# Performance work log

Measured on AMD Instinct MI355X. Metric: run time of the kernel, lower is better.

Reference implementation:

```python
import jax, jax.numpy as jnp
import numpy as np

NTYPES = 2
NATOMS = (512, 512)
N = 1024          # total atoms
NN = 128          # neighbors per type
M = NTYPES * NN   # 256 neighbor slots per atom
D = 25            # last embedding width
FH = 240          # fitting hidden width
B = 8
RMIN, RMAX = 5.8, 6.0


def _embed_mlp(s, W0, b0, W1, b1, W2, b2):
    # DeepMD-style resnet embedding net: 1 -> D -> D -> D, tanh + skip
    h = jnp.tanh(s @ W0 + b0)
    h = h + jnp.tanh(h @ W1 + b1)
    h = h + jnp.tanh(h @ W2 + b2)
    return h


def setup_inputs() -> dict:
    key = jax.random.key(0)
    ks = jax.random.split(key, 20)
    # relative positions; components in [-4.5, 4.5] so |r| spans <5.8, [5.8,6.0), >=6.0
    image_dR = (jax.random.uniform(ks[0], (B, N, NTYPES, NN, 3), jnp.float32) - 0.5) * 9.0
    # 0 == empty neighbor slot (mask = list_neigh > 0); index-1 in [0, N)
    list_neigh = jax.random.randint(ks[1], (B, N, NTYPES, NN), 0, 1025)
    davg = 0.1 * jax.random.normal(ks[2], (NTYPES, M, 4), jnp.float32)
    dstd = jax.random.uniform(ks[3], (NTYPES, M, 4), jnp.float32, 0.5, 1.5)
    P = NTYPES * NTYPES
    eW0 = jax.random.normal(ks[4], (P, 1, D), jnp.float32)
    eb0 = 0.1 * jax.random.normal(ks[5], (P, D), jnp.float32)
    eW1 = jax.random.normal(ks[6], (P, D, D), jnp.float32) / np.sqrt(D)
    eb1 = 0.1 * jax.random.normal(ks[7], (P, D), jnp.float32)
    eW2 = jax.random.normal(ks[8], (P, D, D), jnp.float32) / np.sqrt(D)
    eb2 = 0.1 * jax.random.normal(ks[9], (P, D), jnp.float32)
    fW0 = jax.random.normal(ks[10], (NTYPES, 16 * D, FH), jnp.float32) / np.sqrt(16 * D)
    fb0 = 0.1 * jax.random.normal(ks[11], (NTYPES, FH), jnp.float32)
    fW1 = jax.random.normal(ks[12], (NTYPES, FH, FH), jnp.float32) / np.sqrt(FH)
    fb1 = 0.1 * jax.random.normal(ks[13], (NTYPES, FH), jnp.float32)
    fW2 = jax.random.normal(ks[14], (NTYPES, FH, FH), jnp.float32) / np.sqrt(FH)
    fb2 = 0.1 * jax.random.normal(ks[15], (NTYPES, FH), jnp.float32)
    fW3 = jax.random.normal(ks[16], (NTYPES, FH, 1), jnp.float32) / np.sqrt(FH)
    fb3 = 0.1 * jax.random.normal(ks[17], (NTYPES, 1), jnp.float32)
    ener_shift = 0.01 * jax.random.normal(ks[18], (NTYPES,), jnp.float32)
    return {
        'image_dR': image_dR, 'list_neigh': list_neigh,
        'davg': davg, 'dstd': dstd,
        'eW0': eW0, 'eb0': eb0, 'eW1': eW1, 'eb1': eb1, 'eW2': eW2, 'eb2': eb2,
        'fW0': fW0, 'fb0': fb0, 'fW1': fW1, 'fb1': fb1, 'fW2': fW2, 'fb2': fb2,
        'fW3': fW3, 'fb3': fb3, 'ener_shift': ener_shift,
        'dfeat': jnp.zeros((1,), jnp.float32),
        'Egroup_weight': jnp.zeros((1,), jnp.float32),
        'divider': jnp.ones((1,), jnp.float32),
    }


def _forward(image_dR, list_neigh, davg, dstd,
             eW0, eb0, eW1, eb1, eW2, eb2,
             fW0, fb0, fW1, fb1, fW2, fb2, fW3, fb3, ener_shift):
    dR = image_dR.reshape(B, N, M, 3)
    neigh = list_neigh.reshape(B, N, M)
    mask = neigh > 0
    mf = mask.astype(dR.dtype)
    dR2 = jnp.sum(dR * dR, axis=-1)                       # [B,N,M]
    safe_dR2 = jnp.where(mask, dR2, 1.0)
    Rij = jnp.sqrt(safe_dR2)
    inr = mf / Rij                                        # 1/|r|, 0 off-mask
    x = Rij * mf                                          # nr = dR2/Rij = |r|
    Ri_xyz = dR / safe_dR2[..., None] * mf[..., None]     # r / |r|^2
    inr2 = inr * inr
    inr4 = inr2 * inr2
    inr3 = inr4 * x
    # smooth switching function on [RMIN, RMAX]
    u = (x - RMIN) / (RMAX - RMIN)
    poly = u * u * u * (-6.0 * u * u + 15.0 * u - 10.0) + 1.0
    dpoly = (3.0 * u * u * (-6.0 * u * u + 15.0 * u - 10.0)
             + u * u * u * (-12.0 * u + 15.0)) / (RMAX - RMIN)
    mid = (x >= RMIN) & (x < RMAX)
    vv = jnp.where(x < RMIN, 1.0, jnp.where(mid, poly, 0.0)) * mf
    dvv = jnp.where(mid, dpoly, 0.0) * mf
    Ri_pre = jnp.concatenate([inr[..., None], Ri_xyz], axis=-1)   # [B,N,M,4]
    common = (dvv * inr)[..., None] * dR                          # [B,N,M,3]
    row0 = dR * (inr3 * vv)[..., None] - Ri_pre[..., 0:1] * common
    eye = jnp.eye(3, dtype=dR.dtype)
    outer = (2.0 * dR[..., :, None] * dR[..., None, :] * inr4[..., None, None]
             - eye * inr2[..., None, None])                       # [B,N,M,3,3]
    rows = outer * vv[..., None, None] - Ri_pre[..., 1:4, None] * common[..., None, :]
    Ri_d = jnp.concatenate([row0[..., None, :], rows], axis=-2) * mf[..., None, None]  # [B,N,M,4,3]
    Ri = Ri_pre * vv[..., None]
    # per-type normalization stats broadcast over atoms of each type
    davg_res = jnp.concatenate([jnp.broadcast_to(davg[t], (NATOMS[t], M, 4)) for t in range(NTYPES)], axis=0)
    dstd_res = jnp.concatenate([jnp.broadcast_to(dstd[t], (NATOMS[t], M, 4)) for t in range(NTYPES)], axis=0)
    Ri = (Ri - davg_res) / dstd_res
    Ri_d = Ri_d / dstd_res[..., None]

    def ei_fn(Ri_n):
        Ei_list = []
        start = 0
        for t in range(NTYPES):
            na = NATOMS[t]
            Rt = jax.lax.slice_in_dim(Ri_n, start, start + na, axis=1)  # [B,na,M,4]
            acc = jnp.zeros((B, na, 4, D), Ri_n.dtype)
            for t1 in range(NTYPES):
                p = t * NTYPES + t1
                blk = Rt[:, :, t1 * NN:(t1 + 1) * NN]                  # [B,na,NN,4]
                G = _embed_mlp(blk[..., 0:1], eW0[p], eb0[p], eW1[p], eb1[p], eW2[p], eb2[p])
                acc = acc + jnp.einsum('bnkd,bnke->bnde', blk, G)
            acc = acc * (4.0 / (NN * NTYPES * 4))
            DRt = jnp.einsum('bnde,bndf->bnef', acc, acc[..., :16]).reshape(B, na, D * 16)
            h = jnp.tanh(DRt @ fW0[t] + fb0[t])
            h = h + jnp.tanh(h @ fW1[t] + fb1[t])
            h = h + jnp.tanh(h @ fW2[t] + fb2[t])
            Ei_list.append(h @ fW3[t] + fb3[t] + ener_shift[t])
            start += na
        return jnp.concatenate(Ei_list, axis=1)   # [B,N,1]

    Ei, vjpf = jax.vjp(ei_fn, Ri)
    dE, = vjpf(jnp.ones_like(Ei))                 # dEi/dRi  [B,N,M,4]
    Etot = jnp.sum(Ei, axis=1)                    # [B,1]
    pair = jnp.einsum('bnmd,bnmdx->bnmx', dE, Ri_d)   # per-pair force term [B,N,M,3]
    F_self = -jnp.sum(pair, axis=2)
    j = neigh - 1
    valid = j >= 0
    flat_idx = jnp.where(valid, j, N) + jnp.arange(B)[:, None, None] * (N + 1)
    contrib = jnp.where(valid[..., None], pair, 0.0)
    seg = jax.ops.segment_sum(contrib.reshape(-1, 3), flat_idx.reshape(-1), num_segments=B * (N + 1))
    F = F_self + seg.reshape(B, N + 1, 3)[:, :N]
    return Etot, Ei, F


def reference(image_dR, list_neigh, davg, dstd,
              eW0, eb0, eW1, eb1, eW2, eb2,
              fW0, fb0, fW1, fb1, fW2, fb2, fW3, fb3, ener_shift,
              dfeat, Egroup_weight, divider):
    # dfeat / Egroup_weight / divider are in the torch forward signature but unused
    return _forward(image_dR, list_neigh, davg, dstd,
                    eW0, eb0, eW1, eb1, eW2, eb2,
                    fW0, fb0, fW1, fb1, fW2, fb2, fW3, fb3, ener_shift)
```

## Files before the change

kernel.cpp:

```cpp
#include <hip/hip_runtime.h>

#define DEV __device__ __forceinline__

#define RA(F) F(0) F(1) F(2) F(3) F(4) F(5) F(6) F(7) F(8) F(9) F(10) F(11) \
  F(12) F(13) F(14) F(15) F(16) F(17) F(18) F(19) F(20) F(21) F(22) F(23) F(24)
#define RB(F,j) F(j,0) F(j,1) F(j,2) F(j,3) F(j,4) F(j,5) F(j,6) F(j,7) F(j,8) \
  F(j,9) F(j,10) F(j,11) F(j,12) F(j,13) F(j,14) F(j,15) F(j,16) F(j,17) \
  F(j,18) F(j,19) F(j,20) F(j,21) F(j,22) F(j,23) F(j,24)
#define AP8(F) F(0) F(1) F(2) F(3) F(4) F(5) F(6) F(7)

namespace {

constexpr int B_ = 8;
constexpr int N_ = 1024;
constexpr int M_ = 256;
constexpr int D_ = 25;
constexpr int FH_ = 240;
constexpr int NATOM = B_ * N_;
constexpr float CSC = 1.0f / 256.0f;

DEV float fast_tanh(float x) {
  float ax = fabsf(x);
  float e = __expf(-2.0f * ax);
  float r = (1.0f - e) * __builtin_amdgcn_rcpf(1.0f + e);
  return copysignf(r, x);
}

DEV void geom_blk(float dx, float dy, float dz, int nb, int t, int m,
                  const float* __restrict__ davg, const float* __restrict__ dstd,
                  float& o0, float& o1, float& o2, float& o3) {
  float mf = (nb > 0) ? 1.0f : 0.0f;
  float dr2 = dx * dx + dy * dy + dz * dz;
  float safe = (nb > 0) ? dr2 : 1.0f;
  float rs = __builtin_amdgcn_rsqf(safe);
  float rij = safe * rs;
  float inr = mf * rs;
  float x = rij * mf;
  float inr2 = inr * inr;
  float u = (x - 5.8f) * 5.0f;
  float uu = u * u;
  float A = -6.0f * uu + 15.0f * u - 10.0f;
  float poly = uu * u * A + 1.0f;
  bool mid = (x >= 5.8f) && (x < 6.0f);
  float vv = ((x < 5.8f) ? 1.0f : (mid ? poly : 0.0f)) * mf;
  int bidx = (t * M_ + m) * 4;
  float4 av = *(const float4*)(davg + bidx);
  float4 sv = *(const float4*)(dstd + bidx);
  o0 = (inr * vv - av.x) * __builtin_amdgcn_rcpf(sv.x);
  o1 = (dx * inr2 * vv - av.y) * __builtin_amdgcn_rcpf(sv.y);
  o2 = (dy * inr2 * vv - av.z) * __builtin_amdgcn_rcpf(sv.z);
  o3 = (dz * inr2 * vv - av.w) * __builtin_amdgcn_rcpf(sv.w);
}

DEV void geom_force(float dx, float dy, float dz, int nb, int t, int m,
                    const float* __restrict__ dstd,
                    float dE0, float dE1, float dE2, float dE3,
                    float& px, float& py, float& pz) {
  float mf = (nb > 0) ? 1.0f : 0.0f;
  float dr2 = dx * dx + dy * dy + dz * dz;
  float safe = (nb > 0) ? dr2 : 1.0f;
  float rs = __builtin_amdgcn_rsqf(safe);
  float rij = safe * rs;
  float inr = mf * rs;
  float x = rij * mf;
  float inr2 = inr * inr;
  float inr4 = inr2 * inr2;
  float inr3 = inr4 * x;
  float u = (x - 5.8f) * 5.0f;
  float uu = u * u;
  float A = -6.0f * uu + 15.0f * u - 10.0f;
  float poly = uu * u * A + 1.0f;
  float dpoly = (3.0f * uu * A + uu * u * (-12.0f * u + 15.0f)) * 5.0f;
  bool mid = (x >= 5.8f) && (x < 6.0f);
  float vv = ((x < 5.8f) ? 1.0f : (mid ? poly : 0.0f)) * mf;
  float dvv = (mid ? dpoly : 0.0f) * mf;
  int bidx = (t * M_ + m) * 4;
  float4 sv = *(const float4*)(dstd + bidx);
  float e0 = dE0 * mf * __builtin_amdgcn_rcpf(sv.x);
  float e1 = dE1 * mf * __builtin_amdgcn_rcpf(sv.y);
  float e2 = dE2 * mf * __builtin_amdgcn_rcpf(sv.z);
  float e3 = dE3 * mf * __builtin_amdgcn_rcpf(sv.w);
  float ci = dvv * inr;
  float comx = ci * dx, comy = ci * dy, comz = ci * dz;
  float iv = inr3 * vv;
  float pre0 = inr, pre1 = dx * inr2, pre2 = dy * inr2, pre3 = dz * inr2;
  float txx = 2.0f * dx * dx * inr4 - inr2;
  float tyy = 2.0f * dy * dy * inr4 - inr2;
  float tzz = 2.0f * dz * dz * inr4 - inr2;
  float txy = 2.0f * dx * dy * inr4;
  float txz = 2.0f * dx * dz * inr4;
  float tyz = 2.0f * dy * dz * inr4;
  px = e0 * (dx * iv - pre0 * comx) + e1 * (txx * vv - pre1 * comx) +
       e2 * (txy * vv - pre2 * comx) + e3 * (txz * vv - pre3 * comx);
  py = e0 * (dy * iv - pre0 * comy) + e1 * (txy * vv - pre1 * comy) +
       e2 * (tyy * vv - pre2 * comy) + e3 * (tyz * vv - pre3 * comy);
  pz = e0 * (dz * iv - pre0 * comz) + e1 * (txz * vv - pre1 * comz) +
       e2 * (tyz * vv - pre2 * comz) + e3 * (tzz * vv - pre3 * comz);
}

#define K1H0(e) float h##e = fast_tanh(fmaf(s0, W0p[e], b0p[e]));
#define K1A1(e) float a##e = b1p[e];
#define K1M1E(f,e) a##e = fmaf(hf, W1p[(f)*25+(e)], a##e);
#define K1M1R(f) { const float hf = h##f; RB(K1M1E, f) }
#define K1H1(e) h##e += fast_tanh(a##e);
#define K1A2(e) a##e = b2p[e];
#define K1M2E(f,e) a##e = fmaf(hf, W2p[(f)*25+(e)], a##e);
#define K1M2R(f) { const float hf = h##f; RB(K1M2E, f) }
#define K1ST(e) sGT[e][m] = h##e + fast_tanh(a##e);

__global__ __launch_bounds__(256, 4) void k_embed_acc(
    const float* __restrict__ dR, const int* __restrict__ neigh,
    const float* __restrict__ davg, const float* __restrict__ dstd,
    const float* __restrict__ eW0, const float* __restrict__ eb0,
    const float* __restrict__ eW1, const float* __restrict__ eb1,
    const float* __restrict__ eW2, const float* __restrict__ eb2,
    float* __restrict__ acc_ws) {
  __shared__ float sGT[D_][260];
  __shared__ float sBT[4][260];
  int atom = blockIdx.x;
  int n = atom & (N_ - 1);
  int t = (n >= 512) ? 1 : 0;
  int m = threadIdx.x;
  int p = __builtin_amdgcn_readfirstlane(t * 2 + (m >> 7));
  const float* W0p = eW0 + p * D_;
  const float* b0p = eb0 + p * D_;
  const float* W1p = eW1 + p * 625;
  const float* b1p = eb1 + p * D_;
  const float* W2p = eW2 + p * 625;
  const float* b2p = eb2 + p * D_;
  int base = atom * M_ + m;
  float dx = dR[base * 3 + 0];
  float dy = dR[base * 3 + 1];
  float dz = dR[base * 3 + 2];
  int nb = neigh[base];
  float bb0, bb1, bb2, bb3;
  geom_blk(dx, dy, dz, nb, t, m, davg, dstd, bb0, bb1, bb2, bb3);
  float s0 = bb0;
  RA(K1H0)
  RA(K1A1)
  RA(K1M1R)
  RA(K1H1)
  RA(K1A2)
  RA(K1M2R)
  RA(K1ST)
  sBT[0][m] = bb0; sBT[1][m] = bb1; sBT[2][m] = bb2; sBT[3][m] = bb3;
  __syncthreads();
  if (threadIdx.x < 100) {
    int e = threadIdx.x >> 2;
    int d = threadIdx.x & 3;
    const float4* g4 = (const float4*)(&sGT[e][0]);
    const float4* b4 = (const float4*)(&sBT[d][0]);
    float sum = 0.0f;
    for (int k = 0; k < 64; ++k) {
      float4 g = g4[k];
      float4 b = b4[k];
      sum += b.x * g.x + b.y * g.y + b.z * g.z + b.w * g.w;
    }
    acc_ws[atom * 100 + d * D_ + e] = sum * CSC;
  }
}

#define DECL8(v) float c0=(v),c1=(v),c2=(v),c3=(v),c4=(v),c5=(v),c6=(v),c7=(v);
#define F8X(q)  c##q = fmaf(sX[q][i], w, c##q);
#define F8H0(q) c##q = fmaf(sH0[q][f], w, c##q);
#define F8H1(q) c##q = fmaf(sH1[q][f], w, c##q);
#define F8T2(q) c##q = fmaf(sT2[q][k], w, c##q);
#define F8T1(q) c##q = fmaf(sT1[q][k], w, c##q);
#define F8G0(q) c##q = fmaf(sH0[q][jj], w, c##q);
#define L0S(q) sH0[q][j] = fast_tanh(c##q);
#define L1S(q) { float tv = fast_tanh(c##q); sT1[q][j] = tv; sH1[q][j] = sH0[q][j] + tv; }
#define L2S(q) { float tv = fast_tanh(c##q); sT2[q][j] = tv; atomicAdd(&sEi[q], (sH1[q][j] + tv) * w3); }
#define G2S(q) { float tv = sT2[q][j]; sT2[q][j] = w3 * (1.0f - tv * tv); }
#define D1S(q) { float dh1 = c##q; float tv = sT1[q][j]; sH1[q][j] = dh1; sT1[q][j] = dh1 * (1.0f - tv * tv); }
#define D0S(q) { float h0v = sH0[q][j]; sH0[q][j] = c##q * (1.0f - h0v * h0v); }
#define DXS(q) sX[q][i] = c##q;

__global__ __launch_bounds__(256, 4) void k_fit(
    const float* __restrict__ acc_ws,
    const float* __restrict__ fW0, const float* __restrict__ fb0,
    const float* __restrict__ fW1, const float* __restrict__ fb1,
    const float* __restrict__ fW2, const float* __restrict__ fb2,
    const float* __restrict__ fW3, const float* __restrict__ fb3,
    const float* __restrict__ ener_shift,
    float* __restrict__ dacc_ws, float* __restrict__ out) {
  constexpr int AB = 8;
  __shared__ float sAcc[AB][100];
  __shared__ float sX[AB][400];
  __shared__ float sH0[AB][FH_];
  __shared__ float sT1[AB][FH_];
  __shared__ float sH1[AB][FH_];
  __shared__ float sT2[AB][FH_];
  __shared__ float sEi[AB];
  int a0 = blockIdx.x * AB;
  int bb = a0 >> 10;
  int n0 = a0 & (N_ - 1);
  int t = (n0 >= 512) ? 1 : 0;
  int tid = threadIdx.x;
  for (int idx = tid; idx < AB * 100; idx += 256)
    ((float*)sAcc)[idx] = acc_ws[a0 * 100 + idx];
  if (tid < AB) sEi[tid] = 0.0f;
  __syncthreads();
  for (int idx = tid; idx < AB * 400; idx += 256) {
    int a = idx / 400; int r = idx % 400; int e = r >> 4; int f = r & 15;
    const float* A = sAcc[a];
    sX[a][r] = A[e] * A[f] + A[25 + e] * A[25 + f] + A[50 + e] * A[50 + f] +
               A[75 + e] * A[75 + f];
  }
  __syncthreads();
  const float* W0 = fW0 + t * 400 * FH_;
  const float* W1 = fW1 + t * FH_ * FH_;
  const float* W2 = fW2 + t * FH_ * FH_;
  const float* B0 = fb0 + t * FH_;
  const float* B1 = fb1 + t * FH_;
  const float* B2 = fb2 + t * FH_;
  const float* W3 = fW3 + t * FH_;
  int j = tid;
  if (j < FH_) {
    DECL8(B0[j])
    for (int i = 0; i < 400; ++i) { float w = W0[i * FH_ + j]; AP8(F8X) }
    AP8(L0S)
  }
  __syncthreads();
  if (j < FH_) {
    DECL8(B1[j])
    for (int f = 0; f < FH_; ++f) { float w = W1[f * FH_ + j]; AP8(F8H0) }
    AP8(L1S)
  }
  __syncthreads();
  if (j < FH_) {
    DECL8(B2[j])
    for (int f = 0; f < FH_; ++f) { float w = W2[f * FH_ + j]; AP8(F8H1) }
    float w3 = W3[j];
    AP8(L2S)
  }
  __syncthreads();
  if (tid < AB) {
    float ei = sEi[tid] + fb3[t] + ener_shift[t];
    out[8 + a0 + tid] = ei;
    sEi[tid] = ei;
  }
  if (j < FH_) {
    float w3 = W3[j];
    AP8(G2S)
  }
  __syncthreads();
  if (tid == 0) {
    float s = sEi[0] + sEi[1] + sEi[2] + sEi[3] + sEi[4] + sEi[5] + sEi[6] + sEi[7];
    atomicAdd(&out[bb], s);
  }
  if (j < FH_) {
    DECL8(W3[j])
    for (int k = 0; k < FH_; ++k) { float w = W2[j * FH_ + k]; AP8(F8T2) }
    AP8(D1S)
  }
  __syncthreads();
  if (j < FH_) {
    DECL8(sH1[0][j])
    c1 = sH1[1][j]; c2 = sH1[2][j]; c3 = sH1[3][j];
    c4 = sH1[4][j]; c5 = sH1[5][j]; c6 = sH1[6][j]; c7 = sH1[7][j];
    for (int k = 0; k < FH_; ++k) { float w = W1[j * FH_ + k]; AP8(F8T1) }
    AP8(D0S)
  }
  __syncthreads();
  for (int i = tid; i < 400; i += 256) {
    DECL8(0.0f)
    for (int jj = 0; jj < FH_; ++jj) { float w = W0[i * FH_ + jj]; AP8(F8G0) }
    AP8(DXS)
  }
  __syncthreads();
  for (int idx = tid; idx < AB * 100; idx += 256) {
    int a = idx / 100; int r = idx % 100; int d = r / 25; int e = r % 25;
    const float* A = sAcc[a];
    const float* DX = sX[a];
    float sum = 0.0f;
#pragma unroll
    for (int f = 0; f < 16; ++f) sum = fmaf(DX[e * 16 + f], A[d * 25 + f], sum);
    if (e < 16) {
#pragma unroll
      for (int e2 = 0; e2 < 25; ++e2) sum = fmaf(DX[e2 * 16 + e], A[d * 25 + e2], sum);
    }
    dacc_ws[a0 * 100 + idx] = sum;
  }
}

#define K3H0(e) float x##e = fast_tanh(fmaf(s0, W0p[e], b0p[e]));
#define K3A1(e) float a##e = b1p[e];
#define K3M1E(f,e) a##e = fmaf(hf, W1p[(f)*25+(e)], a##e);
#define K3M1R(f) { const float hf = x##f; RB(K3M1E, f) }
#define K3T1(e) float t##e = fast_tanh(a##e); x##e += t##e;
#define K3A2(e) a##e = b2p[e];
#define K3M2E(f,e) a##e = fmaf(hf, W2p[(f)*25+(e)], a##e);
#define K3M2R(f) { const float hf = x##f; RB(K3M2E, f) }
#define K3DY(e) float y##e;
#define K3SD(e) { float t2 = fast_tanh(a##e); float G = x##e + t2; \
  db0 = fmaf(dacp[e], G, db0); db1 = fmaf(dacp[25+(e)], G, db1); \
  db2 = fmaf(dacp[50+(e)], G, db2); db3 = fmaf(dacp[75+(e)], G, db3); \
  float dg = CSC * (dacp[e] * bb0 + dacp[25+(e)] * bb1 + \
                    dacp[50+(e)] * bb2 + dacp[75+(e)] * bb3); \
  y##e = dg * (1.0f - t2 * t2); a##e = dg; }
#define K3SEF(e,f) s = fmaf(y##f, W2p[(e)*25+(f)], s);
#define K3SE(e) { float s = a##e; RB(K3SEF, e) a##e = s; }
#define K3G1(e) y##e = a##e * (1.0f - t##e * t##e);
#define K3SFF(e,f) s = fmaf(y##f, W1p[(e)*25+(f)], s);
#define K3SF(e) { float s = a##e; RB(K3SFF, e) float h0e = x##e - t##e; \
  dsum = fmaf(s * (1.0f - h0e * h0e), W0p[e], dsum); }

__global__ __launch_bounds__(256, 2) void k_bwd_force(
    const float* __restrict__ dR, const int* __restrict__ neigh,
    const float* __restrict__ davg, const float* __restrict__ dstd,
    const float* __restrict__ eW0, const float* __restrict__ eb0,
    const float* __restrict__ eW1, const float* __restrict__ eb1,
    const float* __restrict__ eW2, const float* __restrict__ eb2,
    const float* __restrict__ dacc_ws, float* __restrict__ out) {
  __shared__ float sF[3];
  int atom = blockIdx.x;
  int bb = atom >> 10;
  int n = atom & (N_ - 1);
  int t = (n >= 512) ? 1 : 0;
  int m = threadIdx.x;
  if (m < 3) sF[m] = 0.0f;
  __syncthreads();
  int p = __builtin_amdgcn_readfirstlane(t * 2 + (m >> 7));
  const float* W0p = eW0 + p * D_;
  const float* b0p = eb0 + p * D_;
  const float* W1p = eW1 + p * 625;
  const float* b1p = eb1 + p * D_;
  const float* W2p = eW2 + p * 625;
  const float* b2p = eb2 + p * D_;
  const float* dacp = dacc_ws + atom * 100;
  int base = atom * M_ + m;
  float dx = dR[base * 3 + 0];
  float dy = dR[base * 3 + 1];
  float dz = dR[base * 3 + 2];
  int nb = neigh[base];
  float bb0, bb1, bb2, bb3;
  geom_blk(dx, dy, dz, nb, t, m, davg, dstd, bb0, bb1, bb2, bb3);
  float s0 = bb0;
  RA(K3H0)
  RA(K3A1)
  RA(K3M1R)
  RA(K3T1)
  RA(K3A2)
  RA(K3M2R)
  RA(K3DY)
  float db0 = 0.0f, db1 = 0.0f, db2 = 0.0f, db3 = 0.0f;
  RA(K3SD)
  RA(K3SE)
  RA(K3G1)
  float dsum = 0.0f;
  RA(K3SF)
  float dE0 = db0 * CSC + dsum;
  float dE1 = db1 * CSC;
  float dE2 = db2 * CSC;
  float dE3 = db3 * CSC;
  float px, py, pz;
  geom_force(dx, dy, dz, nb, t, m, dstd, dE0, dE1, dE2, dE3, px, py, pz);
  float rx = px, ry = py, rz = pz;
#pragma unroll
  for (int off = 32; off > 0; off >>= 1) {
    rx += __shfl_down(rx, off, 64);
    ry += __shfl_down(ry, off, 64);
    rz += __shfl_down(rz, off, 64);
  }
  if ((m & 63) == 0) {
    atomicAdd(&sF[0], rx);
    atomicAdd(&sF[1], ry);
    atomicAdd(&sF[2], rz);
  }
  if (nb > 0) {
    int jn = nb - 1;
    int fi = 8 + NATOM + (bb * N_ + jn) * 3;
    atomicAdd(&out[fi + 0], px);
    atomicAdd(&out[fi + 1], py);
    atomicAdd(&out[fi + 2], pz);
  }
  __syncthreads();
  if (m < 3) atomicAdd(&out[8 + NATOM + atom * 3 + m], -sF[m]);
}

}

extern "C" void kernel_launch(void* const* d_in, const int* in_sizes, int n_in,
                              void* d_out, int out_size, void* d_ws, size_t ws_size,
                              hipStream_t stream) {
  (void)in_sizes; (void)n_in; (void)ws_size;
  const float* image_dR   = (const float*)d_in[0];
  const int*   list_neigh = (const int*)d_in[1];
  const float* davg       = (const float*)d_in[2];
  const float* dstd       = (const float*)d_in[3];
  const float* eW0        = (const float*)d_in[4];
  const float* eb0        = (const float*)d_in[5];
  const float* eW1        = (const float*)d_in[6];
  const float* eb1        = (const float*)d_in[7];
  const float* eW2        = (const float*)d_in[8];
  const float* eb2        = (const float*)d_in[9];
  const float* fW0        = (const float*)d_in[10];
  const float* fb0        = (const float*)d_in[11];
  const float* fW1        = (const float*)d_in[12];
  const float* fb1        = (const float*)d_in[13];
  const float* fW2        = (const float*)d_in[14];
  const float* fb2        = (const float*)d_in[15];
  const float* fW3        = (const float*)d_in[16];
  const float* fb3        = (const float*)d_in[17];
  const float* ener_shift = (const float*)d_in[18];
  float* out = (float*)d_out;
  float* acc_ws  = (float*)d_ws;
  float* dacc_ws = acc_ws + NATOM * 100;

  hipMemsetAsync(d_out, 0, (size_t)out_size * sizeof(float), stream);
  k_embed_acc<<<NATOM, 256, 0, stream>>>(image_dR, list_neigh, davg, dstd,
                                         eW0, eb0, eW1, eb1, eW2, eb2, acc_ws);
  k_fit<<<NATOM / 8, 256, 0, stream>>>(acc_ws, fW0, fb0, fW1, fb1, fW2, fb2,
                                       fW3, fb3, ener_shift, dacc_ws, out);
  k_bwd_force<<<NATOM, 256, 0, stream>>>(image_dR, list_neigh, davg, dstd,
                                         eW0, eb0, eW1, eb1, eW2, eb2,
                                         dacc_ws, out);
}
```

Before: 1.150 ms.

## Run embedding-net matmuls on bf16 MFMA in forward and backward kernels

Replaces the per-thread scalar 25x25 embedding MLP layers, in both the forward accumulation kernel and the backward force kernel, with 16x16x32 bf16 MFMA tiles. Weights are staged into shared memory as padded bf16 matrices, and activations are written to a shared bf16 tile between layers. The descriptor contraction and the dE reductions are reorganised around the MFMA output layout, using cross-lane shuffles. This trades the large FMA and register cost of the unrolled scalar MLP for matrix-core throughput, at the risk of bf16 precision loss in hidden activations and weights, plus extra shared-memory staging per block.

```diff
diff --git a/kernel.cpp b/kernel.cpp
--- a/kernel.cpp
+++ b/kernel.cpp
@@ -2,11 +2,11 @@
 
 #define DEV __device__ __forceinline__
 
-#define RA(F) F(0) F(1) F(2) F(3) F(4) F(5) F(6) F(7) F(8) F(9) F(10) F(11) \
-  F(12) F(13) F(14) F(15) F(16) F(17) F(18) F(19) F(20) F(21) F(22) F(23) F(24)
-#define RB(F,j) F(j,0) F(j,1) F(j,2) F(j,3) F(j,4) F(j,5) F(j,6) F(j,7) F(j,8) \
-  F(j,9) F(j,10) F(j,11) F(j,12) F(j,13) F(j,14) F(j,15) F(j,16) F(j,17) \
-  F(j,18) F(j,19) F(j,20) F(j,21) F(j,22) F(j,23) F(j,24)
+typedef short bf16x8 __attribute__((ext_vector_type(8)));
+typedef float floatx4 __attribute__((ext_vector_type(4)));
+
+#define RC(F) F(0,0) F(0,1) F(1,0) F(1,1) F(2,0) F(2,1) F(3,0) F(3,1)
+#define R4(F) F(0) F(1) F(2) F(3)
 #define AP8(F) F(0) F(1) F(2) F(3) F(4) F(5) F(6) F(7)
 
 namespace {
@@ -18,12 +18,23 @@
 constexpr int FH_ = 240;
 constexpr int NATOM = B_ * N_;
 constexpr float CSC = 1.0f / 256.0f;
+constexpr int XP = 40;
 
 DEV float fast_tanh(float x) {
   float ax = fabsf(x);
   float e = __expf(-2.0f * ax);
   float r = (1.0f - e) * __builtin_amdgcn_rcpf(1.0f + e);
   return copysignf(r, x);
+}
+
+DEV short f2bf(float f) {
+  unsigned u = __builtin_bit_cast(unsigned, f);
+  unsigned r = (u + 0x7FFFu + ((u >> 16) & 1u)) >> 16;
+  return (short)r;
+}
+
+DEV floatx4 mm16(bf16x8 a, bf16x8 b, floatx4 c) {
+  return __builtin_amdgcn_mfma_f32_16x16x32_bf16(a, b, c, 0, 0, 0);
 }
 
 DEV void geom_blk(float dx, float dy, float dz, int nb, int t, int m,
@@ -98,82 +109,148 @@
        e2 * (tyz * vv - pre2 * comz) + e3 * (tzz * vv - pre3 * comz);
 }
 
-#define K1H0(e) float h##e = fast_tanh(fmaf(s0, W0p[e], b0p[e]));
-#define K1A1(e) float a##e = b1p[e];
-#define K1M1E(f,e) a##e = fmaf(hf, W1p[(f)*25+(e)], a##e);
-#define K1M1R(f) { const float hf = h##f; RB(K1M1E, f) }
-#define K1H1(e) h##e += fast_tanh(a##e);
-#define K1A2(e) a##e = b2p[e];
-#define K1M2E(f,e) a##e = fmaf(hf, W2p[(f)*25+(e)], a##e);
-#define K1M2R(f) { const float hf = h##f; RB(K1M2E, f) }
-#define K1ST(e) sGT[e][m] = h##e + fast_tanh(a##e);
-
-__global__ __launch_bounds__(256, 4) void k_embed_acc(
+template <int NMAT>
+DEV void stage_wb(int t, int tid, const float* __restrict__ eW1,
+                  const float* __restrict__ eW2, short* __restrict__ sWB) {
+  for (int idx = tid; idx < 2 * NMAT * 1024; idx += 256) {
+    int h = idx / (NMAT * 1024);
+    int rem = idx - h * (NMAT * 1024);
+    int mat = rem >> 10;
+    int nn = (rem >> 5) & 31;
+    int kk = rem & 31;
+    int p = t * 2 + h;
+    float v = 0.0f;
+    if (nn < 25 && kk < 25) {
+      if (mat == 0)      v = eW1[p * 625 + kk * 25 + nn];
+      else if (mat == 1) v = eW2[p * 625 + kk * 25 + nn];
+      else if (mat == 2) v = eW2[p * 625 + nn * 25 + kk];
+      else               v = eW1[p * 625 + nn * 25 + kk];
+    }
+    sWB[idx] = f2bf(v);
+  }
+}
+
+DEV void stage_b(int t, int tid, const float* __restrict__ eW0,
+                 const float* __restrict__ eb0, const float* __restrict__ eb1,
+                 const float* __restrict__ eb2, float* __restrict__ sB) {
+  if (tid < 200) {
+    int h = tid / 100;
+    int r2 = tid - h * 100;
+    int which = r2 / 25, e = r2 - which * 25;
+    int p = t * 2 + h;
+    float v = (which == 0) ? eW0[p * 25 + e]
+            : (which == 1) ? eb0[p * 25 + e]
+            : (which == 2) ? eb1[p * 25 + e] : eb2[p * 25 + e];
+    sB[tid] = v;
+  }
+}
+
+#define XW(r, ct, val) sX[(mrow + (r)) * XP + (ct) * 16 + lid] = f2bf(val);
+#define H0C(r, ct) float h0_##r##_##ct = fast_tanh(fmaf(bk##r.x, W0f##ct, b0f##ct)); \
+  XW(r, ct, h0_##r##_##ct)
+#define T1C(r, ct) float t1_##r##_##ct = fast_tanh(Dc##ct[r] + b1f##ct); \
+  float h1_##r##_##ct = h0_##r##_##ct + t1_##r##_##ct; XW(r, ct, h1_##r##_##ct)
+#define BF4(v) v += __shfl_xor(v, 1); v += __shfl_xor(v, 2); \
+  v += __shfl_xor(v, 4); v += __shfl_xor(v, 8);
+#define PR2(v) v += __shfl_xor(v, 16); v += __shfl_xor(v, 32);
+#define LDB(name, mat) \
+  bf16x8 name##0 = *(const bf16x8*)&sWB[((half * NMATK + (mat)) * 32 + lid) * 32 + quad * 8]; \
+  bf16x8 name##1 = *(const bf16x8*)&sWB[((half * NMATK + (mat)) * 32 + 16 + lid) * 32 + quad * 8];
+
+__global__ __launch_bounds__(256, 3) void k_embed_acc(
     const float* __restrict__ dR, const int* __restrict__ neigh,
     const float* __restrict__ davg, const float* __restrict__ dstd,
     const float* __restrict__ eW0, const float* __restrict__ eb0,
     const float* __restrict__ eW1, const float* __restrict__ eb1,
     const float* __restrict__ eW2, const float* __restrict__ eb2,
     float* __restrict__ acc_ws) {
-  __shared__ float sGT[D_][260];
-  __shared__ float sBT[4][260];
+  __shared__ short sX[M_ * XP];
+  __shared__ short sWB[2 * 2 * 1024];
+  __shared__ float sB[200];
+  __shared__ float4 sBlk4[M_];
+  __shared__ float sWacc[4][4][32];
   int atom = blockIdx.x;
   int n = atom & (N_ - 1);
   int t = (n >= 512) ? 1 : 0;
-  int m = threadIdx.x;
-  int p = __builtin_amdgcn_readfirstlane(t * 2 + (m >> 7));
-  const float* W0p = eW0 + p * D_;
-  const float* b0p = eb0 + p * D_;
-  const float* W1p = eW1 + p * 625;
-  const float* b1p = eb1 + p * D_;
-  const float* W2p = eW2 + p * 625;
-  const float* b2p = eb2 + p * D_;
-  int base = atom * M_ + m;
-  float dx = dR[base * 3 + 0];
-  float dy = dR[base * 3 + 1];
-  float dz = dR[base * 3 + 2];
-  int nb = neigh[base];
-  float bb0, bb1, bb2, bb3;
-  geom_blk(dx, dy, dz, nb, t, m, davg, dstd, bb0, bb1, bb2, bb3);
-  float s0 = bb0;
-  RA(K1H0)
-  RA(K1A1)
-  RA(K1M1R)
-  RA(K1H1)
-  RA(K1A2)
-  RA(K1M2R)
-  RA(K1ST)
-  sBT[0][m] = bb0; sBT[1][m] = bb1; sBT[2][m] = bb2; sBT[3][m] = bb3;
-  __syncthreads();
-  if (threadIdx.x < 100) {
-    int e = threadIdx.x >> 2;
-    int d = threadIdx.x & 3;
-    const float4* g4 = (const float4*)(&sGT[e][0]);
-    const float4* b4 = (const float4*)(&sBT[d][0]);
-    float sum = 0.0f;
-    for (int k = 0; k < 64; ++k) {
-      float4 g = g4[k];
-      float4 b = b4[k];
-      sum += b.x * g.x + b.y * g.y + b.z * g.z + b.w * g.w;
+  int tid = threadIdx.x;
+  stage_wb<2>(t, tid, eW1, eW2, sWB);
+  stage_b(t, tid, eW0, eb0, eb1, eb2, sB);
+  {
+    int base = atom * M_ + tid;
+    float dx = dR[base * 3 + 0], dy = dR[base * 3 + 1], dz = dR[base * 3 + 2];
+    int nb = neigh[base];
+    float g0, g1, g2, g3;
+    geom_blk(dx, dy, dz, nb, t, tid, davg, dstd, g0, g1, g2, g3);
+    sBlk4[tid] = make_float4(g0, g1, g2, g3);
+  }
+  __syncthreads();
+  const int NMATK = 2;
+  int lane = tid & 63, w = tid >> 6, quad = lane >> 4, lid = lane & 15;
+  int half = w >> 1;
+  int e1i = 16 + lid;
+  bool ev1 = (e1i < 25);
+  const float* Bh = sB + half * 100;
+  float W0f0 = Bh[lid];        float W0f1 = ev1 ? Bh[e1i] : 0.0f;
+  float b0f0 = Bh[25 + lid];   float b0f1 = ev1 ? Bh[25 + e1i] : 0.0f;
+  float b1f0 = Bh[50 + lid];   float b1f1 = ev1 ? Bh[50 + e1i] : 0.0f;
+  float b2f0 = Bh[75 + lid];   float b2f1 = ev1 ? Bh[75 + e1i] : 0.0f;
+  LDB(BW1T, 0) LDB(BW2T, 1)
+  floatx4 Z4 = {0.0f, 0.0f, 0.0f, 0.0f};
+  float pa00 = 0, pa01 = 0, pa10 = 0, pa11 = 0,
+        pa20 = 0, pa21 = 0, pa30 = 0, pa31 = 0;
+#define GAC(r, ct) { float G = h1_##r##_##ct + fast_tanh(Dc##ct[r] + b2f##ct); \
+    pa0##ct = fmaf(bk##r.x, G, pa0##ct); pa1##ct = fmaf(bk##r.y, G, pa1##ct); \
+    pa2##ct = fmaf(bk##r.z, G, pa2##ct); pa3##ct = fmaf(bk##r.w, G, pa3##ct); }
+  for (int rt = 0; rt < 4; ++rt) {
+    int rowbase = ((w << 2) + rt) << 4;
+    int mrow = rowbase + (quad << 2);
+    float4 bk0 = sBlk4[mrow + 0];
+    float4 bk1 = sBlk4[mrow + 1];
+    float4 bk2 = sBlk4[mrow + 2];
+    float4 bk3 = sBlk4[mrow + 3];
+    RC(H0C)
+    const bf16x8* ap = (const bf16x8*)&sX[(rowbase + lid) * XP + quad * 8];
+    bf16x8 af = *ap;
+    floatx4 Dc0 = mm16(af, BW1T0, Z4);
+    floatx4 Dc1 = mm16(af, BW1T1, Z4);
+    RC(T1C)
+    af = *ap;
+    Dc0 = mm16(af, BW2T0, Z4);
+    Dc1 = mm16(af, BW2T1, Z4);
+    RC(GAC)
+  }
+  PR2(pa00) PR2(pa01) PR2(pa10) PR2(pa11)
+  PR2(pa20) PR2(pa21) PR2(pa30) PR2(pa31)
+  if (lane < 16) {
+    sWacc[w][0][lid] = pa00; sWacc[w][1][lid] = pa10;
+    sWacc[w][2][lid] = pa20; sWacc[w][3][lid] = pa30;
+    if (ev1) {
+      sWacc[w][0][e1i] = pa01; sWacc[w][1][e1i] = pa11;
+      sWacc[w][2][e1i] = pa21; sWacc[w][3][e1i] = pa31;
     }
-    acc_ws[atom * 100 + d * D_ + e] = sum * CSC;
+  }
+  __syncthreads();
+  if (tid < 100) {
+    int d = tid / 25, e = tid - d * 25;
+    float s = sWacc[0][d][e] + sWacc[1][d][e] + sWacc[2][d][e] + sWacc[3][d][e];
+    acc_ws[atom * 100 + tid] = s * CSC;
   }
 }
 
 #define DECL8(v) float c0=(v),c1=(v),c2=(v),c3=(v),c4=(v),c5=(v),c6=(v),c7=(v);
-#define F8X(q)  c##q = fmaf(sX[q][i], w, c##q);
-#define F8H0(q) c##q = fmaf(sH0[q][f], w, c##q);
-#define F8H1(q) c##q = fmaf(sH1[q][f], w, c##q);
-#define F8T2(q) c##q = fmaf(sT2[q][k], w, c##q);
-#define F8T1(q) c##q = fmaf(sT1[q][k], w, c##q);
-#define F8G0(q) c##q = fmaf(sH0[q][jj], w, c##q);
+#define F8X(q)  c##q = fmaf(sXf[q][i], wv, c##q);
+#define F8H0(q) c##q = fmaf(sH0[q][f], wv, c##q);
+#define F8H1(q) c##q = fmaf(sH1[q][f], wv, c##q);
+#define F8T2(q) c##q = fmaf(sT2[q][k], wv, c##q);
+#define F8T1(q) c##q = fmaf(sT1[q][k], wv, c##q);
+#define F8G0(q) c##q = fmaf(sH0[q][jj], wv, c##q);
 #define L0S(q) sH0[q][j] = fast_tanh(c##q);
 #define L1S(q) { float tv = fast_tanh(c##q); sT1[q][j] = tv; sH1[q][j] = sH0[q][j] + tv; }
 #define L2S(q) { float tv = fast_tanh(c##q); sT2[q][j] = tv; atomicAdd(&sEi[q], (sH1[q][j] + tv) * w3); }
 #define G2S(q) { float tv = sT2[q][j]; sT2[q][j] = w3 * (1.0f - tv * tv); }
 #define D1S(q) { float dh1 = c##q; float tv = sT1[q][j]; sH1[q][j] = dh1; sT1[q][j] = dh1 * (1.0f - tv * tv); }
 #define D0S(q) { float h0v = sH0[q][j]; sH0[q][j] = c##q * (1.0f - h0v * h0v); }
-#define DXS(q) sX[q][i] = c##q;
+#define DXS(q) sXf[q][i] = c##q;
 
 __global__ __launch_bounds__(256, 4) void k_fit(
     const float* __restrict__ acc_ws,
@@ -185,7 +262,7 @@
     float* __restrict__ dacc_ws, float* __restrict__ out) {
   constexpr int AB = 8;
   __shared__ float sAcc[AB][100];
-  __shared__ float sX[AB][400];
+  __shared__ float sXf[AB][400];
   __shared__ float sH0[AB][FH_];
   __shared__ float sT1[AB][FH_];
   __shared__ float sH1[AB][FH_];
@@ -203,8 +280,8 @@
   for (int idx = tid; idx < AB * 400; idx += 256) {
     int a = idx / 400; int r = idx % 400; int e = r >> 4; int f = r & 15;
     const float* A = sAcc[a];
-    sX[a][r] = A[e] * A[f] + A[25 + e] * A[25 + f] + A[50 + e] * A[50 + f] +
-               A[75 + e] * A[75 + f];
+    sXf[a][r] = A[e] * A[f] + A[25 + e] * A[25 + f] + A[50 + e] * A[50 + f] +
+                A[75 + e] * A[75 + f];
   }
   __syncthreads();
   const float* W0 = fW0 + t * 400 * FH_;
@@ -217,19 +294,19 @@
   int j = tid;
   if (j < FH_) {
     DECL8(B0[j])
-    for (int i = 0; i < 400; ++i) { float w = W0[i * FH_ + j]; AP8(F8X) }
+    for (int i = 0; i < 400; ++i) { float wv = W0[i * FH_ + j]; AP8(F8X) }
     AP8(L0S)
   }
   __syncthreads();
   if (j < FH_) {
     DECL8(B1[j])
-    for (int f = 0; f < FH_; ++f) { float w = W1[f * FH_ + j]; AP8(F8H0) }
+    for (int f = 0; f < FH_; ++f) { float wv = W1[f * FH_ + j]; AP8(F8H0) }
     AP8(L1S)
   }
   __syncthreads();
   if (j < FH_) {
     DECL8(B2[j])
-    for (int f = 0; f < FH_; ++f) { float w = W2[f * FH_ + j]; AP8(F8H1) }
+    for (int f = 0; f < FH_; ++f) { float wv = W2[f * FH_ + j]; AP8(F8H1) }
     float w3 = W3[j];
     AP8(L2S)
   }
@@ -250,7 +327,7 @@
   }
   if (j < FH_) {
     DECL8(W3[j])
-    for (int k = 0; k < FH_; ++k) { float w = W2[j * FH_ + k]; AP8(F8T2) }
+    for (int k = 0; k < FH_; ++k) { float wv = W2[j * FH_ + k]; AP8(F8T2) }
     AP8(D1S)
   }
   __syncthreads();
@@ -258,20 +335,20 @@
     DECL8(sH1[0][j])
     c1 = sH1[1][j]; c2 = sH1[2][j]; c3 = sH1[3][j];
     c4 = sH1[4][j]; c5 = sH1[5][j]; c6 = sH1[6][j]; c7 = sH1[7][j];
-    for (int k = 0; k < FH_; ++k) { float w = W1[j * FH_ + k]; AP8(F8T1) }
+    for (int k = 0; k < FH_; ++k) { float wv = W1[j * FH_ + k]; AP8(F8T1) }
     AP8(D0S)
   }
   __syncthreads();
   for (int i = tid; i < 400; i += 256) {
     DECL8(0.0f)
-    for (int jj = 0; jj < FH_; ++jj) { float w = W0[i * FH_ + jj]; AP8(F8G0) }
+    for (int jj = 0; jj < FH_; ++jj) { float wv = W0[i * FH_ + jj]; AP8(F8G0) }
     AP8(DXS)
   }
   __syncthreads();
   for (int idx = tid; idx < AB * 100; idx += 256) {
     int a = idx / 100; int r = idx % 100; int d = r / 25; int e = r % 25;
     const float* A = sAcc[a];
-    const float* DX = sX[a];
+    const float* DX = sXf[a];
     float sum = 0.0f;
 #pragma unroll
     for (int f = 0; f < 16; ++f) sum = fmaf(DX[e * 16 + f], A[d * 25 + f], sum);
@@ -283,28 +360,6 @@
   }
 }
 
-#define K3H0(e) float x##e = fast_tanh(fmaf(s0, W0p[e], b0p[e]));
-#define K3A1(e) float a##e = b1p[e];
-#define K3M1E(f,e) a##e = fmaf(hf, W1p[(f)*25+(e)], a##e);
-#define K3M1R(f) { const float hf = x##f; RB(K3M1E, f) }
-#define K3T1(e) float t##e = fast_tanh(a##e); x##e += t##e;
-#define K3A2(e) a##e = b2p[e];
-#define K3M2E(f,e) a##e = fmaf(hf, W2p[(f)*25+(e)], a##e);
-#define K3M2R(f) { const float hf = x##f; RB(K3M2E, f) }
-#define K3DY(e) float y##e;
-#define K3SD(e) { float t2 = fast_tanh(a##e); float G = x##e + t2; \
-  db0 = fmaf(dacp[e], G, db0); db1 = fmaf(dacp[25+(e)], G, db1); \
-  db2 = fmaf(dacp[50+(e)], G, db2); db3 = fmaf(dacp[75+(e)], G, db3); \
-  float dg = CSC * (dacp[e] * bb0 + dacp[25+(e)] * bb1 + \
-                    dacp[50+(e)] * bb2 + dacp[75+(e)] * bb3); \
-  y##e = dg * (1.0f - t2 * t2); a##e = dg; }
-#define K3SEF(e,f) s = fmaf(y##f, W2p[(e)*25+(f)], s);
-#define K3SE(e) { float s = a##e; RB(K3SEF, e) a##e = s; }
-#define K3G1(e) y##e = a##e * (1.0f - t##e * t##e);
-#define K3SFF(e,f) s = fmaf(y##f, W1p[(e)*25+(f)], s);
-#define K3SF(e) { float s = a##e; RB(K3SFF, e) float h0e = x##e - t##e; \
-  dsum = fmaf(s * (1.0f - h0e * h0e), W0p[e], dsum); }
-
 __global__ __launch_bounds__(256, 2) void k_bwd_force(
     const float* __restrict__ dR, const int* __restrict__ neigh,
     const float* __restrict__ davg, const float* __restrict__ dstd,
@@ -312,49 +367,103 @@
     const float* __restrict__ eW1, const float* __restrict__ eb1,
     const float* __restrict__ eW2, const float* __restrict__ eb2,
     const float* __restrict__ dacc_ws, float* __restrict__ out) {
+  __shared__ short sX[M_ * XP];
+  __shared__ short sWB[2 * 4 * 1024];
+  __shared__ float sB[200];
+  __shared__ float sDacc[100];
+  __shared__ float4 sBlk4[M_];
+  __shared__ float4 sDE4[M_];
   __shared__ float sF[3];
   int atom = blockIdx.x;
-  int bb = atom >> 10;
+  int bbx = atom >> 10;
   int n = atom & (N_ - 1);
   int t = (n >= 512) ? 1 : 0;
-  int m = threadIdx.x;
-  if (m < 3) sF[m] = 0.0f;
-  __syncthreads();
-  int p = __builtin_amdgcn_readfirstlane(t * 2 + (m >> 7));
-  const float* W0p = eW0 + p * D_;
-  const float* b0p = eb0 + p * D_;
-  const float* W1p = eW1 + p * 625;
-  const float* b1p = eb1 + p * D_;
-  const float* W2p = eW2 + p * 625;
-  const float* b2p = eb2 + p * D_;
-  const float* dacp = dacc_ws + atom * 100;
-  int base = atom * M_ + m;
-  float dx = dR[base * 3 + 0];
-  float dy = dR[base * 3 + 1];
-  float dz = dR[base * 3 + 2];
-  int nb = neigh[base];
-  float bb0, bb1, bb2, bb3;
-  geom_blk(dx, dy, dz, nb, t, m, davg, dstd, bb0, bb1, bb2, bb3);
-  float s0 = bb0;
-  RA(K3H0)
-  RA(K3A1)
-  RA(K3M1R)
-  RA(K3T1)
-  RA(K3A2)
-  RA(K3M2R)
-  RA(K3DY)
-  float db0 = 0.0f, db1 = 0.0f, db2 = 0.0f, db3 = 0.0f;
-  RA(K3SD)
-  RA(K3SE)
-  RA(K3G1)
-  float dsum = 0.0f;
-  RA(K3SF)
-  float dE0 = db0 * CSC + dsum;
-  float dE1 = db1 * CSC;
-  float dE2 = db2 * CSC;
-  float dE3 = db3 * CSC;
+  int tid = threadIdx.x;
+  if (tid < 3) sF[tid] = 0.0f;
+  stage_wb<4>(t, tid, eW1, eW2, sWB);
+  stage_b(t, tid, eW0, eb0, eb1, eb2, sB);
+  if (tid < 100) sDacc[tid] = dacc_ws[atom * 100 + tid];
+  int base = atom * M_ + tid;
+  float dxv = dR[base * 3 + 0], dyv = dR[base * 3 + 1], dzv = dR[base * 3 + 2];
+  int nbv = neigh[base];
+  {
+    float g0, g1, g2, g3;
+    geom_blk(dxv, dyv, dzv, nbv, t, tid, davg, dstd, g0, g1, g2, g3);
+    sBlk4[tid] = make_float4(g0, g1, g2, g3);
+  }
+  __syncthreads();
+  const int NMATK = 4;
+  int lane = tid & 63, w = tid >> 6, quad = lane >> 4, lid = lane & 15;
+  int half = w >> 1;
+  int e1i = 16 + lid;
+  bool ev1 = (e1i < 25);
+  const float* Bh = sB + half * 100;
+  float W0f0 = Bh[lid];        float W0f1 = ev1 ? Bh[e1i] : 0.0f;
+  float b0f0 = Bh[25 + lid];   float b0f1 = ev1 ? Bh[25 + e1i] : 0.0f;
+  float b1f0 = Bh[50 + lid];   float b1f1 = ev1 ? Bh[50 + e1i] : 0.0f;
+  float b2f0 = Bh[75 + lid];   float b2f1 = ev1 ? Bh[75 + e1i] : 0.0f;
+  float da00 = sDacc[lid];      float da01 = ev1 ? sDacc[e1i] : 0.0f;
+  float da10 = sDacc[25 + lid]; float da11 = ev1 ? sDacc[25 + e1i] : 0.0f;
+  float da20 = sDacc[50 + lid]; float da21 = ev1 ? sDacc[50 + e1i] : 0.0f;
+  float da30 = sDacc[75 + lid]; float da31 = ev1 ? sDacc[75 + e1i] : 0.0f;
+  LDB(BW1T, 0) LDB(BW2T, 1) LDB(BW2B, 2) LDB(BW1B, 3)
+  floatx4 Z4 = {0.0f, 0.0f, 0.0f, 0.0f};
+#define T2C(r, ct) float t2_##r##_##ct = fast_tanh(Dc##ct[r] + b2f##ct); \
+    float G_##r##_##ct = h1_##r##_##ct + t2_##r##_##ct; \
+    float dG_##r##_##ct = CSC * (da0##ct * bk##r.x + da1##ct * bk##r.y + \
+                                 da2##ct * bk##r.z + da3##ct * bk##r.w); \
+    XW(r, ct, dG_##r##_##ct * (1.0f - t2_##r##_##ct * t2_##r##_##ct))
+#define DBLK(r) \
+    float db_##r##_0 = da00 * G_##r##_0 + da01 * G_##r##_1; \
+    float db_##r##_1 = da10 * G_##r##_0 + da11 * G_##r##_1; \
+    float db_##r##_2 = da20 * G_##r##_0 + da21 * G_##r##_1; \
+    float db_##r##_3 = da30 * G_##r##_0 + da31 * G_##r##_1;
+#define DBR(r) BF4(db_##r##_0) BF4(db_##r##_1) BF4(db_##r##_2) BF4(db_##r##_3)
+#define DH1C(r, ct) float dh1_##r##_##ct = dG_##r##_##ct + Dc##ct[r]; \
+    XW(r, ct, dh1_##r##_##ct * (1.0f - t1_##r##_##ct * t1_##r##_##ct))
+#define DSC(r) float dh0_##r##_0 = dh1_##r##_0 + Dc0[r]; \
+    float dh0_##r##_1 = dh1_##r##_1 + Dc1[r]; \
+    float ds_##r = dh0_##r##_0 * (1.0f - h0_##r##_0 * h0_##r##_0) * W0f0 \
+                 + dh0_##r##_1 * (1.0f - h0_##r##_1 * h0_##r##_1) * W0f1; \
+    BF4(ds_##r)
+  for (int rt = 0; rt < 4; ++rt) {
+    int rowbase = ((w << 2) + rt) << 4;
+    int mrow = rowbase + (quad << 2);
+    float4 bk0 = sBlk4[mrow + 0];
+    float4 bk1 = sBlk4[mrow + 1];
+    float4 bk2 = sBlk4[mrow + 2];
+    float4 bk3 = sBlk4[mrow + 3];
+    RC(H0C)
+    const bf16x8* ap = (const bf16x8*)&sX[(rowbase + lid) * XP + quad * 8];
+    bf16x8 af = *ap;
+    floatx4 Dc0 = mm16(af, BW1T0, Z4);
+    floatx4 Dc1 = mm16(af, BW1T1, Z4);
+    RC(T1C)
+    af = *ap;
+    Dc0 = mm16(af, BW2T0, Z4);
+    Dc1 = mm16(af, BW2T1, Z4);
+    RC(T2C)
+    R4(DBLK)
+    R4(DBR)
+    af = *ap;
+    Dc0 = mm16(af, BW2B0, Z4);
+    Dc1 = mm16(af, BW2B1, Z4);
+    RC(DH1C)
+    af = *ap;
+    Dc0 = mm16(af, BW1B0, Z4);
+    Dc1 = mm16(af, BW1B1, Z4);
+    R4(DSC)
+    if (lid == 0) {
+      sDE4[mrow + 0] = make_float4(db_0_0 * CSC + ds_0, db_0_1 * CSC, db_0_2 * CSC, db_0_3 * CSC);
+      sDE4[mrow + 1] = make_float4(db_1_0 * CSC + ds_1, db_1_1 * CSC, db_1_2 * CSC, db_1_3 * CSC);
+      sDE4[mrow + 2] = make_float4(db_2_0 * CSC + ds_2, db_2_1 * CSC, db_2_2 * CSC, db_2_3 * CSC);
+      sDE4[mrow + 3] = make_float4(db_3_0 * CSC + ds_3, db_3_1 * CSC, db_3_2 * CSC, db_3_3 * CSC);
+    }
+  }
+  __syncthreads();
+  float4 dE = sDE4[tid];
   float px, py, pz;
-  geom_force(dx, dy, dz, nb, t, m, dstd, dE0, dE1, dE2, dE3, px, py, pz);
+  geom_force(dxv, dyv, dzv, nbv, t, tid, dstd, dE.x, dE.y, dE.z, dE.w, px, py, pz);
   float rx = px, ry = py, rz = pz;
 #pragma unroll
   for (int off = 32; off > 0; off >>= 1) {
@@ -362,20 +471,20 @@
     ry += __shfl_down(ry, off, 64);
     rz += __shfl_down(rz, off, 64);
   }
-  if ((m & 63) == 0) {
+  if ((tid & 63) == 0) {
     atomicAdd(&sF[0], rx);
     atomicAdd(&sF[1], ry);
     atomicAdd(&sF[2], rz);
   }
-  if (nb > 0) {
-    int jn = nb - 1;
-    int fi = 8 + NATOM + (bb * N_ + jn) * 3;
+  if (nbv > 0) {
+    int jn = nbv - 1;
+    int fi = 8 + NATOM + (bbx * N_ + jn) * 3;
     atomicAdd(&out[fi + 0], px);
     atomicAdd(&out[fi + 1], py);
     atomicAdd(&out[fi + 2], pz);
   }
   __syncthreads();
-  if (m < 3) atomicAdd(&out[8 + NATOM + atom * 3 + m], -sF[m]);
+  if (tid < 3) atomicAdd(&out[8 + NATOM + atom * 3 + tid], -sF[tid]);
 }
 
 }
```

Result: faster. 1.107 ms (-3.8%).
